# Kernel optimization log

Measured on AMD Instinct MI355X. Metric: run time of the kernel, lower is better.

Reference implementation:

```python
import jax, jax.numpy as jnp
import numpy as np

B, N, K = 2, 8192, 16
D1, D2, OUT = 128, 256, 128


def setup_inputs() -> dict:
    key = jax.random.key(0)
    ks = jax.random.split(key, 6)
    return {
        "xyz1": jax.random.normal(ks[0], (B, N, 3), dtype=jnp.float32),
        "xyz2": jax.random.normal(ks[1], (B, N, 3), dtype=jnp.float32),
        "points1": jax.random.normal(ks[2], (B, N, D1), dtype=jnp.float32),
        "points2": jax.random.normal(ks[3], (B, N, D2), dtype=jnp.float32),
        # Conv1d(k=1) == pointwise linear: weight [OUT, D1+D2], bias [OUT]
        "W": jax.random.normal(ks[4], (OUT, D1 + D2), dtype=jnp.float32) / np.sqrt(D1 + D2).astype(np.float32),
        "b": jax.random.normal(ks[5], (OUT,), dtype=jnp.float32) * 0.01,
        "nsample": K,
    }


def reference(xyz1, xyz2, points1, points2, W, b, nsample):
    Bb, Nn, _ = xyz1.shape
    # squared pairwise distances, queries=xyz2, keys=xyz1 -> [B, N, N]
    d2 = (jnp.sum(xyz2 * xyz2, -1)[:, :, None]
          + jnp.sum(xyz1 * xyz1, -1)[:, None, :]
          - 2.0 * jnp.einsum('bsc,bnc->bsn', xyz2, xyz1))
    neg_vals, idx = jax.lax.top_k(-d2, nsample)          # K nearest
    dists = -neg_vals                                     # [B, N, K] sq dists
    recip = 1.0 / (dists + 1e-8)
    weight = recip / jnp.sum(recip, axis=2, keepdims=True)  # inverse-dist weights
    # gather neighbor features from points2: [B, N, K, D2]
    g = jnp.take_along_axis(points2, idx.reshape(Bb, Nn * nsample)[:, :, None], axis=1)
    g = g.reshape(Bb, Nn, nsample, -1)
    interp = jnp.sum(g * weight[..., None], axis=2)       # [B, N, D2]
    cat = jnp.concatenate([points1, interp], axis=-1)     # [B, N, D1+D2]
    # Conv1d(kernel=1) over channel dim
    return jnp.einsum('bnc,oc->bno', cat, W) + b
```

## Files before the change

### kernel.cpp

```cpp
#include <hip/hip_runtime.h>
#include <stdint.h>

#define BQ   2
#define NQ   8192
#define D1Q  128
#define D2Q  256
#define OUTQ 128
#define CATQ 384
#define KQ   16

#define NBIN 4096
#define RED_MARGIN 1e-3f
#define LB_MARGIN  1e-2f

#define WREG 6448

#define WS_WFH   0
#define WS_WFL   98304
#define WS_SPXYZ 262144
#define WS_QSXYZ 524288
#define WS_SPIDX 786432
#define WS_QSIDX 819200
#define WS_GBLO  851968
#define WS_GBHI  856064

__device__ __forceinline__ ushort f2bf(float f) {
    uint32_t u = __float_as_uint(f);
    return (ushort)((u + 0x7FFFu + ((u >> 16) & 1u)) >> 16);
}
__device__ __forceinline__ float bf2f(ushort h) {
    return __uint_as_float((uint32_t)h << 16);
}

__device__ __forceinline__ uint32_t encf(float f) {
    uint32_t b = __float_as_uint(f);
    return b ^ (0x80000000u | (uint32_t)((int32_t)b >> 31));
}
__device__ __forceinline__ float decf(uint32_t u) {
    uint32_t bits = (u & 0x80000000u) ? (u ^ 0x80000000u) : ~u;
    return __uint_as_float(bits);
}

__device__ __forceinline__ uint32_t mbcnt64(uint64_t m) {
    return __builtin_amdgcn_mbcnt_hi((uint32_t)(m >> 32),
           __builtin_amdgcn_mbcnt_lo((uint32_t)m, 0u));
}

typedef __attribute__((ext_vector_type(8))) short short8v;
typedef __attribute__((ext_vector_type(4))) float f32x4v;

__device__ __forceinline__ int mort_bin(float x, float y, float z) {
    int bx = (int)((x + 5.0f) * 1.6f); bx = bx < 0 ? 0 : (bx > 15 ? 15 : bx);
    int by = (int)((y + 5.0f) * 1.6f); by = by < 0 ? 0 : (by > 15 ? 15 : by);
    int bz = (int)((z + 5.0f) * 1.6f); bz = bz < 0 ? 0 : (bz > 15 ? 15 : bz);
    int k = 0;
    #pragma unroll
    for (int t = 0; t < 4; ++t)
        k |= (((bx >> t) & 1) << (3 * t)) | (((by >> t) & 1) << (3 * t + 1)) |
             (((bz >> t) & 1) << (3 * t + 2));
    return k;
}

__global__ __launch_bounds__(1024) void prep_all_kernel(
        const float* __restrict__ W,
        ushort* __restrict__ Wfh, ushort* __restrict__ Wfl,
        const float* __restrict__ xyz1, const float* __restrict__ xyz2,
        float4* __restrict__ sp_xyzn, float4* __restrict__ qs_xyzw,
        ushort* __restrict__ sp_idx, ushort* __restrict__ qs_idx,
        float4* __restrict__ gblo, float4* __restrict__ gbhi) {
    __shared__ uint32_t hist[NBIN];
    __shared__ uint32_t sc[16];
    __shared__ uint32_t ab[128 * 8];

    const int bid = blockIdx.x;
    const int tid = threadIdx.x;

    if (bid >= 4) {
        int flat = (bid - 4) * 1024 + tid;
        if (flat < CATQ * OUTQ) {
            int r    = flat & 7;
            int lane = (flat >> 3) & 63;
            int ctk  = flat >> 9;
            int ct   = ctk & 7;
            int kt   = ctk >> 3;
            int o = ct * 16 + (lane & 15);
            int k = kt * 32 + (lane >> 4) * 8 + r;
            float v  = W[o * CATQ + k];
            ushort h = f2bf(v);
            Wfh[flat] = h;
            Wfl[flat] = f2bf(v - bf2f(h));
        }
        return;
    }

    const int  batch = bid & 1;
    const bool isPts = bid < 2;
    const float* src = (isPts ? xyz1 : xyz2) + (size_t)batch * NQ * 3;

    #pragma unroll
    for (int i = tid; i < NBIN; i += 1024) hist[i] = 0u;
    if (isPts) ab[tid] = ((tid & 7) >= 4) ? 0u : 0xFFFFFFFFu;
    __syncthreads();

    float x[8], y[8], z[8];
    int   bin[8];
    #pragma unroll
    for (int e = 0; e < 8; ++e) {
        int idx = e * 1024 + tid;
        const float* p = src + (size_t)idx * 3;
        x[e] = p[0]; y[e] = p[1]; z[e] = p[2];
        bin[e] = mort_bin(x[e], y[e], z[e]);
        atomicAdd(&hist[bin[e]], 1u);
    }
    __syncthreads();

    uint32_t v0 = hist[4 * tid], v1 = hist[4 * tid + 1],
             v2 = hist[4 * tid + 2], v3 = hist[4 * tid + 3];
    uint32_t s = v0 + v1 + v2 + v3;
    uint32_t incl = s;
    #pragma unroll
    for (int d = 1; d < 64; d <<= 1) {
        uint32_t t = __shfl_up(incl, d, 64);
        if ((tid & 63) >= d) incl += t;
    }
    if ((tid & 63) == 63) sc[tid >> 6] = incl;
    __syncthreads();
    if (tid < 16) {
        uint32_t v = sc[tid];
        uint32_t i2 = v;
        #pragma unroll
        for (int d = 1; d < 16; d <<= 1) {
            uint32_t t = __shfl_up(i2, d, 64);
            if (tid >= d) i2 += t;
        }
        sc[tid] = i2 - v;
    }
    __syncthreads();
    uint32_t excl = sc[tid >> 6] + (incl - s);
    hist[4 * tid]     = excl;
    hist[4 * tid + 1] = excl + v0;
    hist[4 * tid + 2] = excl + v0 + v1;
    hist[4 * tid + 3] = excl + v0 + v1 + v2;
    __syncthreads();

    #pragma unroll
    for (int e = 0; e < 8; ++e) {
        int idx = e * 1024 + tid;
        uint32_t pos = atomicAdd(&hist[bin[e]], 1u);
        float n;
        {
            #pragma clang fp contract(off)
            float px = x[e] * x[e], py = y[e] * y[e], pz = z[e] * z[e];
            n = (px + py) + pz;
        }
        if (isPts) {
            sp_xyzn[batch * NQ + pos] = make_float4(x[e], y[e], z[e], n);
            sp_idx[batch * NQ + pos]  = (ushort)idx;
            uint32_t* gw = ab + ((pos >> 6) << 3);
            atomicMin(&gw[0], encf(x[e]));
            atomicMin(&gw[1], encf(y[e]));
            atomicMin(&gw[2], encf(z[e]));
            atomicMax(&gw[4], encf(x[e]));
            atomicMax(&gw[5], encf(y[e]));
            atomicMax(&gw[6], encf(z[e]));
        } else {
            qs_xyzw[batch * NQ + pos] = make_float4(x[e], y[e], z[e], n);
            qs_idx[batch * NQ + pos]  = (ushort)idx;
        }
    }
    if (isPts) {
        __syncthreads();
        if (tid < 128) {
            gblo[batch * 128 + tid] = make_float4(
                decf(ab[tid * 8 + 0]), decf(ab[tid * 8 + 1]),
                decf(ab[tid * 8 + 2]), 0.f);
            gbhi[batch * 128 + tid] = make_float4(
                decf(ab[tid * 8 + 4]), decf(ab[tid * 8 + 5]),
                decf(ab[tid * 8 + 6]), 0.f);
        }
    }
}

__device__ __forceinline__ float npy_d2(float4 pt, float qx, float qy, float qz,
                                        float s2) {
    #pragma clang fp contract(off)
    float d0  = pt.x * qx;
    float dot = fmaf(pt.y, qy, d0);
    dot       = fmaf(pt.z, qz, dot);
    float tt  = s2 + pt.w;
    return tt - 2.0f * dot;
}

__device__ __forceinline__ float red_r(float4 pt, float qx, float qy, float qz) {
    float dot = fmaf(pt.z, qz, fmaf(pt.y, qy, pt.x * qx));
    return fmaf(-2.0f, dot, pt.w);
}

__device__ __forceinline__ uint64_t sort64(uint64_t x, int lane) {
    #pragma unroll
    for (int k = 2; k <= 64; k <<= 1) {
        #pragma unroll
        for (int j = k >> 1; j > 0; j >>= 1) {
            uint64_t p = __shfl_xor((unsigned long long)x, j, 64);
            bool keep_min = (((lane & j) == 0) == ((lane & k) == 0));
            bool pless    = p < x;
            x = (pless == keep_min) ? p : x;
        }
    }
    return x;
}

__global__ __launch_bounds__(256, 4) void fused_kernel(
        const float4* __restrict__ sp_xyzn, const ushort* __restrict__ sp_idx,
        const float4* __restrict__ qs_xyzw, const ushort* __restrict__ qs_idx,
        const float* __restrict__ points1, const float* __restrict__ points2,
        const ushort* __restrict__ Wfh, const ushort* __restrict__ Wfl,
        const float* __restrict__ bias,
        const float4* __restrict__ gblo, const float4* __restrict__ gbhi,
        float* __restrict__ out) {
    __shared__ __align__(16) char smem[4 * WREG + 32];
    ushort* qsl = (ushort*)(smem + 4 * WREG);

    const int tid   = threadIdx.x;
    const int lane  = tid & 63;
    const int w     = tid >> 6;
    const int blk   = (blockIdx.x & 7) * 128 + (blockIdx.x >> 3);
    const int b     = blk >> 9;
    const int qslot = (blk & 511) * 16;

    char*     myreg   = smem + w * WREG;
    uint64_t* wball_w = (uint64_t*)myreg;
    ushort*   sl      = (ushort*)(myreg + 4096);

    if (tid < 16) qsl[tid] = qs_idx[b * NQ + qslot + tid];

    float qx[4], qy[4], qz[4], s2[4];
    int   oqi[4];
    #pragma unroll
    for (int j = 0; j < 4; ++j) {
        float4 q = qs_xyzw[(size_t)b * NQ + qslot + w * 4 + j];
        qx[j] = q.x; qy[j] = q.y; qz[j] = q.z; s2[j] = q.w;
        oqi[j] = (int)qs_idx[b * NQ + qslot + w * 4 + j];
    }

    const float4* spb = sp_xyzn + (size_t)b * NQ;
    const ushort* spi = sp_idx  + (size_t)b * NQ;

    int wstart = qslot + 8 - 512;
    if (wstart < 0) wstart = 0;
    if (wstart > NQ - 1024) wstart = NQ - 1024;
    wstart &= ~63;
    const float4* win = spb + wstart;

    float mn[4];
    #pragma unroll
    for (int j = 0; j < 4; ++j) mn[j] = __uint_as_float(0x7F800000u);

    #pragma unroll 8
    for (int s = 0; s < 16; ++s) {
        float4 pt = win[s * 64 + lane];
        #pragma unroll
        for (int j = 0; j < 4; ++j)
            mn[j] = fminf(mn[j], red_r(pt, qx[j], qy[j], qz[j]));
    }

    float that[4];
    #pragma unroll
    for (int j = 0; j < 4; ++j) {
        float x = mn[j];
        #pragma unroll
        for (int k = 2; k <= 64; k <<= 1) {
            #pragma unroll
            for (int jj = k >> 1; jj > 0; jj >>= 1) {
                float px = __shfl_xor(x, jj, 64);
                bool keep_min = (((lane & jj) == 0) == ((lane & k) == 0));
                float mnv = fminf(x, px), mxv = fmaxf(x, px);
                x = keep_min ? mnv : mxv;
            }
        }
        that[j] = s2[j] + __shfl(x, 15, 64) + RED_MARGIN;
    }

    int scnt_w = 0;
    {
        float qlx = fminf(fminf(qx[0], qx[1]), fminf(qx[2], qx[3]));
        float qly = fminf(fminf(qy[0], qy[1]), fminf(qy[2], qy[3]));
        float qlz = fminf(fminf(qz[0], qz[1]), fminf(qz[2], qz[3]));
        float qhx = fmaxf(fmaxf(qx[0], qx[1]), fmaxf(qx[2], qx[3]));
        float qhy = fmaxf(fmaxf(qy[0], qy[1]), fmaxf(qy[2], qy[3]));
        float qhz = fmaxf(fmaxf(qz[0], qz[1]), fmaxf(qz[2], qz[3]));
        float tmax = fmaxf(fmaxf(that[0], that[1]), fmaxf(that[2], that[3]))
                   + LB_MARGIN;
        #pragma unroll
        for (int h = 0; h < 2; ++h) {
            int g = h * 64 + lane;
            float4 gl = gblo[b * 128 + g];
            float4 gh = gbhi[b * 128 + g];
            float dx = fmaxf(fmaxf(qlx - gh.x, gl.x - qhx), 0.f);
            float dy = fmaxf(fmaxf(qly - gh.y, gl.y - qhy), 0.f);
            float dz = fmaxf(fmaxf(qlz - gh.z, gl.z - qhz), 0.f);
            float lb = dx * dx;
            lb = fmaf(dy, dy, lb);
            lb = fmaf(dz, dz, lb);
            bool sv = (lb <= tmax);
            uint64_t m = __ballot((int)sv);
            if (sv) sl[scnt_w + mbcnt64(m)] = (ushort)g;
            scnt_w += (int)__popcll(m);
        }
    }

    uint32_t cnt[4] = {0u, 0u, 0u, 0u};
    {
        float4 ptA = make_float4(0.f, 0.f, 0.f, 0.f), ptB = ptA;
        uint32_t pA = 0u, pB = 0u;
        if (scnt_w > 0) {
            int g = (int)sl[0];
            ptA = spb[g * 64 + lane]; pA = (uint32_t)spi[g * 64 + lane];
        }
        if (scnt_w > 1) {
            int g = (int)sl[1];
            ptB = spb[g * 64 + lane]; pB = (uint32_t)spi[g * 64 + lane];
        }
        for (int i = 0; i < scnt_w; ++i) {
            float4   pt   = ptA;
            uint32_t pidx = pA;
            ptA = ptB; pA = pB;
            if (i + 2 < scnt_w) {
                int g = (int)sl[i + 2];
                ptB = spb[g * 64 + lane];
                pB  = (uint32_t)spi[g * 64 + lane];
            }
            #pragma unroll
            for (int j = 0; j < 4; ++j) {
                float d2 = npy_d2(pt, qx[j], qy[j], qz[j], s2[j]);
                bool  v  = (d2 <= that[j]);
                uint64_t mask = __ballot((int)v);
                if (mask != 0ull) {
                    if (v) {
                        uint32_t pos    = cnt[j] + mbcnt64(mask);
                        uint32_t bits   = __float_as_uint(d2);
                        uint32_t mapped = bits ^ (0x80000000u |
                                          (uint32_t)((int32_t)bits >> 31));
                        if (pos < 128u)
                            wball_w[j * 128 + pos] =
                                ((uint64_t)mapped << 32) | (uint64_t)pidx;
                    }
                    cnt[j] += (uint32_t)__popcll(mask);
                }
            }
        }
    }

    int   myidxA[4];
    float mywgtA[4];
    #pragma unroll
    for (int j = 0; j < 4; ++j) {
        const uint64_t* wb = wball_w + (size_t)j * 128;
        const uint32_t c = cnt[j];
        uint64_t mykey;
        if (c <= 64u) {
            uint64_t k0 = (lane < (int)c) ? wb[lane] : ~0ull;
            mykey = sort64(k0, lane);
        } else {
            uint32_t cc = c > 128u ? 128u : c;
            uint64_t k0 = wb[lane];
            uint64_t k1 = (lane + 64 < (int)cc) ? wb[lane + 64] : ~0ull;
            k0 = sort64(k0, lane);
            k1 = sort64(k1, lane);
            uint64_t t1 = __shfl((unsigned long long)k1, lane & 15, 64);
            uint64_t km = (lane < 16) ? k0 : ((lane < 32) ? t1 : ~0ull);
            mykey = sort64(km, lane);
        }
        uint32_t mhi   = (uint32_t)(mykey >> 32);
        uint32_t rbits = (mhi & 0x80000000u) ? (mhi ^ 0x80000000u) : ~mhi;
        float    d2w   = __uint_as_float(rbits);
        myidxA[j] = (int)(uint32_t)(mykey & 0xFFFFFFFFull);
        float recip = (lane < KQ) ? (1.0f / (d2w + 1e-8f)) : 0.0f;
        float tot = recip;
        #pragma unroll
        for (int sh = 1; sh < 16; sh <<= 1) tot += __shfl_xor(tot, sh, 64);
        mywgtA[j] = recip / tot;
    }


    ushort* ch = (ushort*)myreg;
    ushort* cl = (ushort*)(myreg + 3136);
    const float* p2b = points2 + (size_t)b * NQ * D2Q;
    #pragma unroll
    for (int j = 0; j < 4; ++j) {
        if (lane < 32) {
            float4 p = ((const float4*)(points1 +
                        (size_t)(b * NQ + oqi[j]) * D1Q))[lane];
            ushort4 hv, lv;
            hv.x = f2bf(p.x); lv.x = f2bf(p.x - bf2f(hv.x));
            hv.y = f2bf(p.y); lv.y = f2bf(p.y - bf2f(hv.y));
            hv.z = f2bf(p.z); lv.z = f2bf(p.z - bf2f(hv.z));
            hv.w = f2bf(p.w); lv.w = f2bf(p.w - bf2f(hv.w));
            *(ushort4*)&ch[j * 392 + lane * 4] = hv;
            *(ushort4*)&cl[j * 392 + lane * 4] = lv;
        }
        float4 acc = make_float4(0.f, 0.f, 0.f, 0.f);
        #pragma unroll
        for (int k = 0; k < KQ; ++k) {
            int   kk = __builtin_amdgcn_readlane(myidxA[j], k);
            float wk = __uint_as_float((uint32_t)__builtin_amdgcn_readlane(
                           (int)__float_as_uint(mywgtA[j]), k));
            float4 row = ((const float4*)(p2b + (size_t)kk * D2Q))[lane];
            acc.x = fmaf(wk, row.x, acc.x);
            acc.y = fmaf(wk, row.y, acc.y);
            acc.z = fmaf(wk, row.z, acc.z);
            acc.w = fmaf(wk, row.w, acc.w);
        }
        {
            ushort4 hv, lv;
            hv.x = f2bf(acc.x); lv.x = f2bf(acc.x - bf2f(hv.x));
            hv.y = f2bf(acc.y); lv.y = f2bf(acc.y - bf2f(hv.y));
            hv.z = f2bf(acc.z); lv.z = f2bf(acc.z - bf2f(hv.z));
            hv.w = f2bf(acc.w); lv.w = f2bf(acc.w - bf2f(hv.w));
            *(ushort4*)&ch[j * 392 + D1Q + lane * 4] = hv;
            *(ushort4*)&cl[j * 392 + D1Q + lane * 4] = lv;
        }
    }
    __syncthreads();

    {
        const int arow = lane & 15;
        const int koff = (lane >> 4) * 8;
        const int ct0  = w * 2;
        const char* rowb = smem + (arow >> 2) * WREG + (arow & 3) * 784;
        f32x4v acc0 = {0.f, 0.f, 0.f, 0.f};
        f32x4v acc1 = {0.f, 0.f, 0.f, 0.f};
        #pragma unroll 4
        for (int kt = 0; kt < 12; ++kt) {
            short8v ah = *(const short8v*)(rowb + (kt * 32 + koff) * 2);
            short8v al = *(const short8v*)(rowb + 3136 + (kt * 32 + koff) * 2);
            const ushort* bhp = Wfh + ((size_t)(kt * 8 + ct0) * 64 + lane) * 8;
            const ushort* blp = Wfl + ((size_t)(kt * 8 + ct0) * 64 + lane) * 8;
            short8v bh0 = *(const short8v*)bhp;
            short8v bl0 = *(const short8v*)blp;
            short8v bh1 = *(const short8v*)(bhp + 512);
            short8v bl1 = *(const short8v*)(blp + 512);
            acc0 = __builtin_amdgcn_mfma_f32_16x16x32_bf16(ah, bh0, acc0, 0, 0, 0);
            acc0 = __builtin_amdgcn_mfma_f32_16x16x32_bf16(al, bh0, acc0, 0, 0, 0);
            acc0 = __builtin_amdgcn_mfma_f32_16x16x32_bf16(ah, bl0, acc0, 0, 0, 0);
            acc1 = __builtin_amdgcn_mfma_f32_16x16x32_bf16(ah, bh1, acc1, 0, 0, 0);
            acc1 = __builtin_amdgcn_mfma_f32_16x16x32_bf16(al, bh1, acc1, 0, 0, 0);
            acc1 = __builtin_amdgcn_mfma_f32_16x16x32_bf16(ah, bl1, acc1, 0, 0, 0);
        }
        const int col0   = ct0 * 16 + (lane & 15);
        const int r0slot = (lane >> 4) * 4;
        const float bv0 = bias[col0];
        const float bv1 = bias[col0 + 16];
        #pragma unroll
        for (int r = 0; r < 4; ++r) {
            int oq = (int)qsl[r0slot + r];
            size_t rowoff = (size_t)(b * NQ + oq) * OUTQ;
            out[rowoff + col0]      = acc0[r] + bv0;
            out[rowoff + col0 + 16] = acc1[r] + bv1;
        }
    }
}

extern "C" void kernel_launch(void* const* d_in, const int* in_sizes, int n_in,
                              void* d_out, int out_size, void* d_ws, size_t ws_size,
                              hipStream_t stream) {
    const float* xyz1    = (const float*)d_in[0];
    const float* xyz2    = (const float*)d_in[1];
    const float* points1 = (const float*)d_in[2];
    const float* points2 = (const float*)d_in[3];
    const float* W       = (const float*)d_in[4];
    const float* bias    = (const float*)d_in[5];

    char* ws = (char*)d_ws;
    ushort*   Wfh     = (ushort*)(ws + WS_WFH);
    ushort*   Wfl     = (ushort*)(ws + WS_WFL);
    float4*   sp_xyzn = (float4*)(ws + WS_SPXYZ);
    float4*   qs_xyzw = (float4*)(ws + WS_QSXYZ);
    ushort*   sp_idx  = (ushort*)(ws + WS_SPIDX);
    ushort*   qs_idx  = (ushort*)(ws + WS_QSIDX);
    float4*   gblo    = (float4*)(ws + WS_GBLO);
    float4*   gbhi    = (float4*)(ws + WS_GBHI);

    prep_all_kernel<<<52, 1024, 0, stream>>>(W, Wfh, Wfl, xyz1, xyz2,
                                             sp_xyzn, qs_xyzw, sp_idx, qs_idx,
                                             gblo, gbhi);
    fused_kernel<<<(BQ * NQ) / 16, 256, 0, stream>>>(
        sp_xyzn, sp_idx, qs_xyzw, qs_idx, points1, points2,
        Wfh, Wfl, bias, gblo, gbhi, (float*)d_out);
}
```

Measured before the change: 150.4 us.

## Split each 16-query block across eight waves with two queries per wave

The fused kernel now runs 512 threads per block, and each of the eight waves handles 2 queries instead of 4. The per-wave shared-memory region, candidate buffers and concatenated-row staging are halved to match. In the final MFMA projection each wave now computes a single 16-column output tile instead of two. The aim is more latency hiding and shorter serial work per wave, since each wave's query bounding box is tighter and fewer grid cells pass the culling test. In exchange, the coarse window-minimum scan and cell culling are repeated by twice as many waves. The tighter launch bounds may also force register spilling.

Result: no change. 150.6 us (+0.2%).

```diff
diff --git a/kernel.cpp b/kernel.cpp
--- a/kernel.cpp
+++ b/kernel.cpp
@@ -13,7 +13,7 @@
 #define RED_MARGIN 1e-3f
 #define LB_MARGIN  1e-2f
 
-#define WREG 6448
+#define WREG 3152
 
 #define WS_WFH   0
 #define WS_WFL   98304
@@ -210,7 +210,7 @@
     return x;
 }
 
-__global__ __launch_bounds__(256, 4) void fused_kernel(
+__global__ __launch_bounds__(512, 8) void fused_kernel(
         const float4* __restrict__ sp_xyzn, const ushort* __restrict__ sp_idx,
         const float4* __restrict__ qs_xyzw, const ushort* __restrict__ qs_idx,
         const float* __restrict__ points1, const float* __restrict__ points2,
@@ -218,8 +218,8 @@
         const float* __restrict__ bias,
         const float4* __restrict__ gblo, const float4* __restrict__ gbhi,
         float* __restrict__ out) {
-    __shared__ __align__(16) char smem[4 * WREG + 32];
-    ushort* qsl = (ushort*)(smem + 4 * WREG);
+    __shared__ __align__(16) char smem[8 * WREG + 32];
+    ushort* qsl = (ushort*)(smem + 8 * WREG);
 
     const int tid   = threadIdx.x;
     const int lane  = tid & 63;
@@ -230,17 +230,17 @@
 
     char*     myreg   = smem + w * WREG;
     uint64_t* wball_w = (uint64_t*)myreg;
-    ushort*   sl      = (ushort*)(myreg + 4096);
+    ushort*   sl      = (ushort*)(myreg + 2048);
 
     if (tid < 16) qsl[tid] = qs_idx[b * NQ + qslot + tid];
 
-    float qx[4], qy[4], qz[4], s2[4];
-    int   oqi[4];
-    #pragma unroll
-    for (int j = 0; j < 4; ++j) {
-        float4 q = qs_xyzw[(size_t)b * NQ + qslot + w * 4 + j];
+    float qx[2], qy[2], qz[2], s2[2];
+    int   oqi[2];
+    #pragma unroll
+    for (int j = 0; j < 2; ++j) {
+        float4 q = qs_xyzw[(size_t)b * NQ + qslot + w * 2 + j];
         qx[j] = q.x; qy[j] = q.y; qz[j] = q.z; s2[j] = q.w;
-        oqi[j] = (int)qs_idx[b * NQ + qslot + w * 4 + j];
+        oqi[j] = (int)qs_idx[b * NQ + qslot + w * 2 + j];
     }
 
     const float4* spb = sp_xyzn + (size_t)b * NQ;
@@ -252,21 +252,21 @@
     wstart &= ~63;
     const float4* win = spb + wstart;
 
-    float mn[4];
-    #pragma unroll
-    for (int j = 0; j < 4; ++j) mn[j] = __uint_as_float(0x7F800000u);
+    float mn[2];
+    #pragma unroll
+    for (int j = 0; j < 2; ++j) mn[j] = __uint_as_float(0x7F800000u);
 
     #pragma unroll 8
     for (int s = 0; s < 16; ++s) {
         float4 pt = win[s * 64 + lane];
         #pragma unroll
-        for (int j = 0; j < 4; ++j)
+        for (int j = 0; j < 2; ++j)
             mn[j] = fminf(mn[j], red_r(pt, qx[j], qy[j], qz[j]));
     }
 
-    float that[4];
-    #pragma unroll
-    for (int j = 0; j < 4; ++j) {
+    float that[2];
+    #pragma unroll
+    for (int j = 0; j < 2; ++j) {
         float x = mn[j];
         #pragma unroll
         for (int k = 2; k <= 64; k <<= 1) {
@@ -283,14 +283,13 @@
 
     int scnt_w = 0;
     {
-        float qlx = fminf(fminf(qx[0], qx[1]), fminf(qx[2], qx[3]));
-        float qly = fminf(fminf(qy[0], qy[1]), fminf(qy[2], qy[3]));
-        float qlz = fminf(fminf(qz[0], qz[1]), fminf(qz[2], qz[3]));
-        float qhx = fmaxf(fmaxf(qx[0], qx[1]), fmaxf(qx[2], qx[3]));
-        float qhy = fmaxf(fmaxf(qy[0], qy[1]), fmaxf(qy[2], qy[3]));
-        float qhz = fmaxf(fmaxf(qz[0], qz[1]), fmaxf(qz[2], qz[3]));
-        float tmax = fmaxf(fmaxf(that[0], that[1]), fmaxf(that[2], that[3]))
-                   + LB_MARGIN;
+        float qlx = fminf(qx[0], qx[1]);
+        float qly = fminf(qy[0], qy[1]);
+        float qlz = fminf(qz[0], qz[1]);
+        float qhx = fmaxf(qx[0], qx[1]);
+        float qhy = fmaxf(qy[0], qy[1]);
+        float qhz = fmaxf(qz[0], qz[1]);
+        float tmax = fmaxf(that[0], that[1]) + LB_MARGIN;
         #pragma unroll
         for (int h = 0; h < 2; ++h) {
             int g = h * 64 + lane;
@@ -309,7 +308,7 @@
         }
     }
 
-    uint32_t cnt[4] = {0u, 0u, 0u, 0u};
+    uint32_t cnt[2] = {0u, 0u};
     {
         float4 ptA = make_float4(0.f, 0.f, 0.f, 0.f), ptB = ptA;
         uint32_t pA = 0u, pB = 0u;
@@ -331,7 +330,7 @@
                 pB  = (uint32_t)spi[g * 64 + lane];
             }
             #pragma unroll
-            for (int j = 0; j < 4; ++j) {
+            for (int j = 0; j < 2; ++j) {
                 float d2 = npy_d2(pt, qx[j], qy[j], qz[j], s2[j]);
                 bool  v  = (d2 <= that[j]);
                 uint64_t mask = __ballot((int)v);
@@ -351,10 +350,10 @@
         }
     }
 
-    int   myidxA[4];
-    float mywgtA[4];
-    #pragma unroll
-    for (int j = 0; j < 4; ++j) {
+    int   myidxA[2];
+    float mywgtA[2];
+    #pragma unroll
+    for (int j = 0; j < 2; ++j) {
         const uint64_t* wb = wball_w + (size_t)j * 128;
         const uint32_t c = cnt[j];
         uint64_t mykey;
@@ -384,10 +383,10 @@
 
 
     ushort* ch = (ushort*)myreg;
-    ushort* cl = (ushort*)(myreg + 3136);
+    ushort* cl = (ushort*)(myreg + 1568);
     const float* p2b = points2 + (size_t)b * NQ * D2Q;
     #pragma unroll
-    for (int j = 0; j < 4; ++j) {
+    for (int j = 0; j < 2; ++j) {
         if (lane < 32) {
             float4 p = ((const float4*)(points1 +
                         (size_t)(b * NQ + oqi[j]) * D1Q))[lane];
@@ -426,37 +425,29 @@
     {
         const int arow = lane & 15;
         const int koff = (lane >> 4) * 8;
-        const int ct0  = w * 2;
-        const char* rowb = smem + (arow >> 2) * WREG + (arow & 3) * 784;
+        const int ct   = w;
+        const char* rowb = smem + (arow >> 1) * WREG + (arow & 1) * 784;
         f32x4v acc0 = {0.f, 0.f, 0.f, 0.f};
-        f32x4v acc1 = {0.f, 0.f, 0.f, 0.f};
         #pragma unroll 4
         for (int kt = 0; kt < 12; ++kt) {
             short8v ah = *(const short8v*)(rowb + (kt * 32 + koff) * 2);
-            short8v al = *(const short8v*)(rowb + 3136 + (kt * 32 + koff) * 2);
-            const ushort* bhp = Wfh + ((size_t)(kt * 8 + ct0) * 64 + lane) * 8;
-            const ushort* blp = Wfl + ((size_t)(kt * 8 + ct0) * 64 + lane) * 8;
+            short8v al = *(const short8v*)(rowb + 1568 + (kt * 32 + koff) * 2);
+            const ushort* bhp = Wfh + ((size_t)(kt * 8 + ct) * 64 + lane) * 8;
+            const ushort* blp = Wfl + ((size_t)(kt * 8 + ct) * 64 + lane) * 8;
             short8v bh0 = *(const short8v*)bhp;
             short8v bl0 = *(const short8v*)blp;
-            short8v bh1 = *(const short8v*)(bhp + 512);
-            short8v bl1 = *(const short8v*)(blp + 512);
             acc0 = __builtin_amdgcn_mfma_f32_16x16x32_bf16(ah, bh0, acc0, 0, 0, 0);
             acc0 = __builtin_amdgcn_mfma_f32_16x16x32_bf16(al, bh0, acc0, 0, 0, 0);
             acc0 = __builtin_amdgcn_mfma_f32_16x16x32_bf16(ah, bl0, acc0, 0, 0, 0);
-            acc1 = __builtin_amdgcn_mfma_f32_16x16x32_bf16(ah, bh1, acc1, 0, 0, 0);
-            acc1 = __builtin_amdgcn_mfma_f32_16x16x32_bf16(al, bh1, acc1, 0, 0, 0);
-            acc1 = __builtin_amdgcn_mfma_f32_16x16x32_bf16(ah, bl1, acc1, 0, 0, 0);
-        }
-        const int col0   = ct0 * 16 + (lane & 15);
+        }
+        const int col0   = ct * 16 + (lane & 15);
         const int r0slot = (lane >> 4) * 4;
         const float bv0 = bias[col0];
-        const float bv1 = bias[col0 + 16];
         #pragma unroll
         for (int r = 0; r < 4; ++r) {
             int oq = (int)qsl[r0slot + r];
             size_t rowoff = (size_t)(b * NQ + oq) * OUTQ;
-            out[rowoff + col0]      = acc0[r] + bv0;
-            out[rowoff + col0 + 16] = acc1[r] + bv1;
+            out[rowoff + col0] = acc0[r] + bv0;
         }
     }
 }
@@ -484,7 +475,7 @@
     prep_all_kernel<<<52, 1024, 0, stream>>>(W, Wfh, Wfl, xyz1, xyz2,
                                              sp_xyzn, qs_xyzw, sp_idx, qs_idx,
                                              gblo, gbhi);
-    fused_kernel<<<(BQ * NQ) / 16, 256, 0, stream>>>(
+    fused_kernel<<<(BQ * NQ) / 16, 512, 0, stream>>>(
         sp_xyzn, sp_idx, qs_xyzw, qs_idx, points1, points2,
         Wfh, Wfl, bias, gblo, gbhi, (float*)d_out);
 }
```
